# Kernel optimization log

Hardware: AMD Instinct MI355X
Metric: run time of the kernel (lower is better)

## Reference

```python
import jax, jax.numpy as jnp
import numpy as np
from itertools import combinations

NDIM = 256
BATCH = 65536


def setup_inputs() -> dict:
    key = jax.random.key(0)
    k1, k2 = jax.random.split(key)
    pairs = np.array(list(combinations(range(NDIM), 2)), dtype=np.int32)  # [comb(ndim,2), 2]
    return {
        "x": jax.random.normal(k1, (BATCH, NDIM), dtype=jnp.float32),
        "rots": jax.random.normal(k2, (pairs.shape[0],), dtype=jnp.float32),
        "idx_i": jnp.asarray(pairs[:, 0]),
        "idx_j": jnp.asarray(pairs[:, 1]),
    }


def _build_mat(rots, idx_i, idx_j, ndim):
    # Equivalent to mat = R_last @ ... @ R_first @ I, then return mat.T.
    # Each Givens rotation R_(i,j,theta) only mixes rows i and j, so we update
    # two rows per step (O(ndim) work) instead of a dense ndim x ndim matmul.
    # Torch uses cfloat, but all imaginary parts are identically zero, so
    # float32 computes the same math.
    def step(mat, t):
        i, j, theta = t
        c = jnp.cos(theta)
        s = jnp.sin(theta)
        ri = mat[i]
        rj = mat[j]
        mat = mat.at[i].set(c * ri - s * rj)
        mat = mat.at[j].set(s * ri + c * rj)
        return mat, None

    mat0 = jnp.eye(ndim, dtype=rots.dtype)
    mat, _ = jax.lax.scan(step, mat0, (idx_i, idx_j, rots))
    return mat.T  # forward does x @ mat.T


def reference(x, rots, idx_i, idx_j):
    m = _build_mat(rots, idx_i, idx_j, x.shape[-1])  # [ndim, ndim]
    return x @ m
```

## Files before the change

### kernel.cpp

```cpp
#include <hip/hip_runtime.h>
#include <hip/hip_bf16.h>
#include <math.h>

#define NDIM 256
#define NROT 32640
#define NSEG 64
#define SEGLEN 510
#define MATE (NDIM * NDIM)
#define NODEE (2 * MATE)

typedef __bf16 bf16x4_t __attribute__((ext_vector_type(4)));
typedef __bf16 bf16x8_t __attribute__((ext_vector_type(8)));
typedef float f32x4_t __attribute__((ext_vector_type(4)));


#define ROT1(RJ, CS) { float nri_ = fmaf((CS).x, ri, -((CS).y * (RJ))); \
                       (RJ) = fmaf((CS).y, ri, (CS).x * (RJ)); ri = nri_; }

#define LOAD16(P, JB, KK) \
    P##0 = *(const f32x4_t*)&tile[(JB)][t][0]; \
    P##1 = *(const f32x4_t*)&tile[(JB)][t][4]; \
    P##2 = *(const f32x4_t*)&tile[(JB) + 1][t][0]; \
    P##3 = *(const f32x4_t*)&tile[(JB) + 1][t][4]; \
    _Pragma("unroll") \
    for (int u = 0; u < 16; u++) P##c[u] = csl[(KK) + u];

#define COMP16(P, JB) \
    _Pragma("unroll") \
    for (int u = 0; u < 4; u++) ROT1(P##0[u], P##c[u]) \
    _Pragma("unroll") \
    for (int u = 0; u < 4; u++) ROT1(P##1[u], P##c[4 + u]) \
    _Pragma("unroll") \
    for (int u = 0; u < 4; u++) ROT1(P##2[u], P##c[8 + u]) \
    _Pragma("unroll") \
    for (int u = 0; u < 4; u++) ROT1(P##3[u], P##c[12 + u]) \
    *(f32x4_t*)&tile[(JB)][t][0] = P##0; \
    *(f32x4_t*)&tile[(JB)][t][4] = P##1; \
    *(f32x4_t*)&tile[(JB) + 1][t][0] = P##2; \
    *(f32x4_t*)&tile[(JB) + 1][t][4] = P##3;

__global__ __launch_bounds__(64, 1) void k_build(const float* __restrict__ rots,
                                                 __bf16* __restrict__ leaves) {
    __shared__ float tile[32][64][8];
    __shared__ float2 csl[SEGLEN + 16];
    const int t = threadIdx.x;
    const int seg = blockIdx.x >> 2;
    const int cg = blockIdx.x & 3;
    const int col = cg * 64 + t;
    const int kg0 = seg * SEGLEN;

    for (int u = t; u < SEGLEN; u += 64) {
        float th = rots[kg0 + u];
        float s, c;
        sincosf(th, &s, &c);
        csl[u] = make_float2(c, s);
    }
    for (int u = SEGLEN + t; u < SEGLEN + 16; u += 64) csl[u] = make_float2(1.f, 0.f);

    #pragma unroll
    for (int jb = 0; jb < 32; jb++) {
        f32x4_t z0 = {0.f, 0.f, 0.f, 0.f}, z1 = {0.f, 0.f, 0.f, 0.f};
        if ((col >> 3) == jb) {
            if ((col & 7) < 4) z0[col & 3] = 1.0f;
            else               z1[col & 3] = 1.0f;
        }
        *(f32x4_t*)&tile[jb][t][0] = z0;
        *(f32x4_t*)&tile[jb][t][4] = z1;
    }

    int k = 0;
    int i = 0, cum = 0;
    while (cum + (NDIM - 1 - i) <= kg0) { cum += NDIM - 1 - i; i++; }
    int j = i + 1 + (kg0 - cum);

    float* T = &tile[0][0][0];
    #define TADDR(r) ((((r) >> 3) * 512) + t * 8 + ((r) & 7))

    while (k < SEGLEN) {
        float ri = T[TADDR(i)];
        int rem = min(NDIM - j, SEGLEN - k);

        int npeel = min((8 - (j & 7)) & 7, rem);
        for (int u = 0; u < npeel; u++) {
            float2 cs = csl[k];
            float rj = T[TADDR(j)];
            float nri = fmaf(cs.x, ri, -(cs.y * rj));
            T[TADDR(j)] = fmaf(cs.y, ri, cs.x * rj);
            ri = nri; j++; k++;
        }
        rem -= npeel;

        if (rem >= 16) {
            int jb = j >> 3;
            f32x4_t A0, A1, A2, A3, B0, B1, B2, B3;
            float2 Ac[16], Bc[16];
            LOAD16(A, jb, k)
            while (rem >= 48) {
                LOAD16(B, jb + 2, k + 16)
                COMP16(A, jb)
                jb += 2; j += 16; k += 16; rem -= 16;
                LOAD16(A, jb + 2, k + 16)
                COMP16(B, jb)
                jb += 2; j += 16; k += 16; rem -= 16;
            }
            if (rem >= 32) {
                LOAD16(B, jb + 2, k + 16)
                COMP16(A, jb)
                jb += 2; j += 16; k += 16; rem -= 16;
                COMP16(B, jb)
                jb += 2; j += 16; k += 16; rem -= 16;
            } else {
                COMP16(A, jb)
                jb += 2; j += 16; k += 16; rem -= 16;
            }
        }

        if (rem >= 8) {
            int jb = j >> 3;
            f32x4_t a0 = *(const f32x4_t*)&tile[jb][t][0];
            f32x4_t a1 = *(const f32x4_t*)&tile[jb][t][4];
            float2 cc[8];
            #pragma unroll
            for (int u = 0; u < 8; u++) cc[u] = csl[k + u];
            #pragma unroll
            for (int u = 0; u < 4; u++) ROT1(a0[u], cc[u])
            #pragma unroll
            for (int u = 0; u < 4; u++) ROT1(a1[u], cc[4 + u])
            *(f32x4_t*)&tile[jb][t][0] = a0;
            *(f32x4_t*)&tile[jb][t][4] = a1;
            j += 8; k += 8; rem -= 8;
        }

        while (rem > 0) {
            float2 cs = csl[k];
            float rj = T[TADDR(j)];
            float nri = fmaf(cs.x, ri, -(cs.y * rj));
            T[TADDR(j)] = fmaf(cs.y, ri, cs.x * rj);
            ri = nri; j++; k++; rem--;
        }

        T[TADDR(i)] = ri;
        if (j == NDIM) { i++; j = i + 1; }
    }
    #undef TADDR

    __bf16* hi = leaves + (size_t)seg * NODEE;
    __bf16* lo = hi + MATE;
    if (seg & 1) {
        for (int jb = 0; jb < 32; jb++) {
            f32x4_t v0 = *(const f32x4_t*)&tile[jb][t][0];
            f32x4_t v1 = *(const f32x4_t*)&tile[jb][t][4];
            #pragma unroll
            for (int u = 0; u < 8; u++) {
                float v = (u < 4) ? v0[u & 3] : v1[u & 3];
                __bf16 h = (__bf16)v;
                hi[(size_t)(jb * 8 + u) * NDIM + col] = h;
                lo[(size_t)(jb * 8 + u) * NDIM + col] = (__bf16)(v - (float)h);
            }
        }
    } else {
        for (int jb = 0; jb < 32; jb++) {
            f32x4_t v0 = *(const f32x4_t*)&tile[jb][t][0];
            f32x4_t v1 = *(const f32x4_t*)&tile[jb][t][4];
            bf16x8_t vh, vl;
            #pragma unroll
            for (int u = 0; u < 8; u++) {
                float v = (u < 4) ? v0[u & 3] : v1[u & 3];
                __bf16 h = (__bf16)v;
                vh[u] = h;
                vl[u] = (__bf16)(v - (float)h);
            }
            *(bf16x8_t*)&hi[(size_t)col * NDIM + jb * 8] = vh;
            *(bf16x8_t*)&lo[(size_t)col * NDIM + jb * 8] = vl;
        }
    }
}

#define LDK 264
__global__ __launch_bounds__(256) void k_combine(const __bf16* __restrict__ src,
                                                 __bf16* __restrict__ dst,
                                                 int finalLevel) {
    __shared__ __bf16 planes[4][64 * LDK];

    const int p = blockIdx.x >> 4;
    const int qd = blockIdx.x & 15;
    const int rbq = (qd >> 2) * 64;
    const int cbq = (qd & 3) * 64;
    const __bf16* A = src + (size_t)(2 * p) * NODEE;
    const __bf16* B = src + (size_t)(2 * p + 1) * NODEE;
    __bf16* Chi = dst + (size_t)p * NODEE;
    __bf16* Clo = Chi + MATE;
    const bool storeT = (!finalLevel) && ((p & 1) == 0);

    const int t = threadIdx.x;
    const int wid = t >> 6, lane = t & 63;
    const int wr2 = (wid >> 1) * 32, wc2 = (wid & 1) * 32;
    const int lrow = lane & 15, kg = lane >> 4;

    const __bf16* plane_src[4] = {B, B + MATE, A, A + MATE};
    const int plane_row0[4] = {rbq, rbq, cbq, cbq};
    #pragma unroll
    for (int q = 0; q < 32; q++) {
        int g = q * 256 + t;
        int pl = g >> 11;
        int c = g & 2047;
        int row = c >> 5, sg = c & 31;
        bf16x8_t v = *(const bf16x8_t*)&plane_src[pl][(size_t)(plane_row0[pl] + row) * NDIM + sg * 8];
        *(bf16x8_t*)&planes[pl][row * LDK + sg * 8] = v;
    }
    __syncthreads();

    f32x4_t acc[2][2] = {};
    #pragma unroll
    for (int kc = 0; kc < 8; kc++) {
        bf16x8_t afh[2], afl[2], bfh[2], bfl[2];
        #pragma unroll
        for (int mt = 0; mt < 2; mt++) {
            int r = (wr2 + mt * 16 + lrow) * LDK + kc * 32 + kg * 8;
            afh[mt] = *(const bf16x8_t*)&planes[0][r];
            afl[mt] = *(const bf16x8_t*)&planes[1][r];
        }
        #pragma unroll
        for (int nt = 0; nt < 2; nt++) {
            int r = (wc2 + nt * 16 + lrow) * LDK + kc * 32 + kg * 8;
            bfh[nt] = *(const bf16x8_t*)&planes[2][r];
            bfl[nt] = *(const bf16x8_t*)&planes[3][r];
        }
        #pragma unroll
        for (int mt = 0; mt < 2; mt++)
            #pragma unroll
            for (int nt = 0; nt < 2; nt++) {
                acc[mt][nt] = __builtin_amdgcn_mfma_f32_16x16x32_bf16(afh[mt], bfh[nt], acc[mt][nt], 0, 0, 0);
                acc[mt][nt] = __builtin_amdgcn_mfma_f32_16x16x32_bf16(afh[mt], bfl[nt], acc[mt][nt], 0, 0, 0);
                acc[mt][nt] = __builtin_amdgcn_mfma_f32_16x16x32_bf16(afl[mt], bfh[nt], acc[mt][nt], 0, 0, 0);
            }
    }

    #pragma unroll
    for (int mt = 0; mt < 2; mt++)
        #pragma unroll
        for (int nt = 0; nt < 2; nt++) {
            int grow = rbq + wr2 + mt * 16 + kg * 4;
            int gcol = cbq + wc2 + nt * 16 + lrow;
            if (storeT) {
                bf16x4_t vh, vl;
                #pragma unroll
                for (int r = 0; r < 4; r++) {
                    float v = acc[mt][nt][r];
                    __bf16 h = (__bf16)v;
                    vh[r] = h;
                    vl[r] = (__bf16)(v - (float)h);
                }
                *(bf16x4_t*)&Chi[(size_t)gcol * NDIM + grow] = vh;
                *(bf16x4_t*)&Clo[(size_t)gcol * NDIM + grow] = vl;
            } else if (finalLevel) {
                #pragma unroll
                for (int r = 0; r < 4; r++)
                    Chi[(size_t)(grow + r) * NDIM + gcol] = (__bf16)acc[mt][nt][r];
            } else {
                #pragma unroll
                for (int r = 0; r < 4; r++) {
                    float v = acc[mt][nt][r];
                    __bf16 h = (__bf16)v;
                    Chi[(size_t)(grow + r) * NDIM + gcol] = h;
                    Clo[(size_t)(grow + r) * NDIM + gcol] = (__bf16)(v - (float)h);
                }
            }
        }
}

#define LDA 72
__global__ __launch_bounds__(256, 2) void k_gemm(const float* __restrict__ X,
                                                 const __bf16* __restrict__ Mhi,
                                                 float* __restrict__ Y) {
    __shared__ __bf16 As[128 * LDA];
    __shared__ __bf16 Bs[128 * LDA];
    const int bx = blockIdx.x;
    const int xcd = bx & 7;
    const int q = bx >> 3;
    const int bn = (q & 1) * 128;
    const int bm = (xcd + (q >> 1) * 8) * 128;
    const int t = threadIdx.x;
    const int wid = t >> 6;
    const int lane = t & 63;
    const int wr = (wid >> 1) * 64;
    const int wc = (wid & 1) * 64;
    const int lrow = lane & 15;
    const int kg = lane >> 4;

    f32x4_t acc[4][4] = {};

    f32x4_t ra[8];
    bf16x8_t rb[4];

    #pragma unroll
    for (int qq = 0; qq < 8; qq++) {
        int g = qq * 256 + t;
        ra[qq] = *(const f32x4_t*)&X[(size_t)(bm + (g >> 4)) * 256 + (g & 15) * 4];
    }
    #pragma unroll
    for (int qq = 0; qq < 4; qq++) {
        int g = qq * 256 + t;
        rb[qq] = *(const bf16x8_t*)&Mhi[(size_t)(bn + (g >> 3)) * 256 + (g & 7) * 8];
    }

    #pragma unroll
    for (int it = 0; it < 4; it++) {
        #pragma unroll
        for (int qq = 0; qq < 8; qq++) {
            int g = qq * 256 + t;
            f32x4_t v = ra[qq];
            bf16x4_t h = {(__bf16)v.x, (__bf16)v.y, (__bf16)v.z, (__bf16)v.w};
            *(bf16x4_t*)&As[(g >> 4) * LDA + (g & 15) * 4] = h;
        }
        #pragma unroll
        for (int qq = 0; qq < 4; qq++) {
            int g = qq * 256 + t;
            *(bf16x8_t*)&Bs[(g >> 3) * LDA + (g & 7) * 8] = rb[qq];
        }
        __syncthreads();

        if (it < 3) {
            int kc = (it + 1) * 64;
            #pragma unroll
            for (int qq = 0; qq < 8; qq++) {
                int g = qq * 256 + t;
                ra[qq] = *(const f32x4_t*)&X[(size_t)(bm + (g >> 4)) * 256 + kc + (g & 15) * 4];
            }
            #pragma unroll
            for (int qq = 0; qq < 4; qq++) {
                int g = qq * 256 + t;
                rb[qq] = *(const bf16x8_t*)&Mhi[(size_t)(bn + (g >> 3)) * 256 + kc + (g & 7) * 8];
            }
        }

        #pragma unroll
        for (int k2 = 0; k2 < 2; k2++) {
            bf16x8_t af[4], bfr[4];
            #pragma unroll
            for (int mt = 0; mt < 4; mt++)
                af[mt] = *(const bf16x8_t*)&As[(wr + mt * 16 + lrow) * LDA + k2 * 32 + kg * 8];
            #pragma unroll
            for (int nt = 0; nt < 4; nt++)
                bfr[nt] = *(const bf16x8_t*)&Bs[(wc + nt * 16 + lrow) * LDA + k2 * 32 + kg * 8];
            #pragma unroll
            for (int mt = 0; mt < 4; mt++)
                #pragma unroll
                for (int nt = 0; nt < 4; nt++)
                    acc[mt][nt] = __builtin_amdgcn_mfma_f32_16x16x32_bf16(af[mt], bfr[nt], acc[mt][nt], 0, 0, 0);
        }
        __syncthreads();
    }

    const int ocol = bn + wc + lrow;
    const int orow = bm + wr + kg * 4;
    #pragma unroll
    for (int mt = 0; mt < 4; mt++)
        #pragma unroll
        for (int nt = 0; nt < 4; nt++)
            #pragma unroll
            for (int r = 0; r < 4; r++)
                Y[(size_t)(orow + mt * 16 + r) * 256 + ocol + nt * 16] = acc[mt][nt][r];
}

extern "C" void kernel_launch(void* const* d_in, const int* in_sizes, int n_in,
                              void* d_out, int out_size, void* d_ws, size_t ws_size,
                              hipStream_t stream) {
    const float* x = (const float*)d_in[0];
    const float* rots = (const float*)d_in[1];
    float* out = (float*)d_out;

    __bf16* B0 = (__bf16*)d_ws;
    __bf16* B1 = B0 + (size_t)NSEG * NODEE;

    k_build<<<NSEG * 4, 64, 0, stream>>>(rots, B0);
    k_combine<<<32 * 16, 256, 0, stream>>>(B0, B1, 0);
    k_combine<<<16 * 16, 256, 0, stream>>>(B1, B0, 0);
    k_combine<<<8 * 16, 256, 0, stream>>>(B0, B1, 0);
    k_combine<<<4 * 16, 256, 0, stream>>>(B1, B0, 0);
    k_combine<<<2 * 16, 256, 0, stream>>>(B0, B1, 0);
    k_combine<<<1 * 16, 256, 0, stream>>>(B1, B0, 1);
    k_gemm<<<1024, 256, 0, stream>>>(x, B0, out);
}
```

Before: 222.5 us.

## Merge tree combine levels into one cooperative kernel with grid sync

Replaces six separate k_combine launches with a single cooperative kernel of 256 blocks that loops over the tree levels and separates them with grid.sync. The aim is to remove the per-launch overhead and the gaps between small, serial launches in the later levels. In exchange, the first level now runs 512 tiles on 256 blocks, so each block does two tiles in turn. The grid-wide barrier also adds its own cost.

After: 572.5 us. +157.3%, slower.

```diff
diff --git a/kernel.cpp b/kernel.cpp
--- a/kernel.cpp
+++ b/kernel.cpp
@@ -1,6 +1,9 @@
 #include <hip/hip_runtime.h>
 #include <hip/hip_bf16.h>
+#include <hip/hip_cooperative_groups.h>
 #include <math.h>
+
+namespace cg = cooperative_groups;
 
 #define NDIM 256
 #define NROT 32640
@@ -45,8 +48,8 @@
     __shared__ float2 csl[SEGLEN + 16];
     const int t = threadIdx.x;
     const int seg = blockIdx.x >> 2;
-    const int cg = blockIdx.x & 3;
-    const int col = cg * 64 + t;
+    const int cg_ = blockIdx.x & 3;
+    const int col = cg_ * 64 + t;
     const int kg0 = seg * SEGLEN;
 
     for (int u = t; u < SEGLEN; u += 64) {
@@ -177,13 +180,12 @@
 }
 
 #define LDK 264
-__global__ __launch_bounds__(256) void k_combine(const __bf16* __restrict__ src,
-                                                 __bf16* __restrict__ dst,
-                                                 int finalLevel) {
-    __shared__ __bf16 planes[4][64 * LDK];
-
-    const int p = blockIdx.x >> 4;
-    const int qd = blockIdx.x & 15;
+
+__device__ __forceinline__ void combine_tile(int p, int qd,
+                                             const __bf16* __restrict__ src,
+                                             __bf16* __restrict__ dst,
+                                             int finalLevel,
+                                             __bf16 (&planes)[4][64 * LDK]) {
     const int rbq = (qd >> 2) * 64;
     const int cbq = (qd & 3) * 64;
     const __bf16* A = src + (size_t)(2 * p) * NODEE;
@@ -269,6 +271,25 @@
         }
 }
 
+__global__ __launch_bounds__(256, 1) void k_tree(__bf16* B0, __bf16* B1) {
+    __shared__ __bf16 planes[4][64 * LDK];
+    cg::grid_group grid = cg::this_grid();
+
+    #pragma unroll 1
+    for (int lv = 0; lv < 6; lv++) {
+        const __bf16* src = (lv & 1) ? (const __bf16*)B1 : (const __bf16*)B0;
+        __bf16* dst = (lv & 1) ? B0 : B1;
+        const int np = NSEG >> (lv + 1);
+        const int njobs = np * 16;
+        for (int job = blockIdx.x; job < njobs; job += gridDim.x) {
+            combine_tile(job >> 4, job & 15, src, dst, lv == 5, planes);
+            __syncthreads();
+        }
+        __threadfence();
+        grid.sync();
+    }
+}
+
 #define LDA 72
 __global__ __launch_bounds__(256, 2) void k_gemm(const float* __restrict__ X,
                                                  const __bf16* __restrict__ Mhi,
@@ -374,11 +395,9 @@
     __bf16* B1 = B0 + (size_t)NSEG * NODEE;
 
     k_build<<<NSEG * 4, 64, 0, stream>>>(rots, B0);
-    k_combine<<<32 * 16, 256, 0, stream>>>(B0, B1, 0);
-    k_combine<<<16 * 16, 256, 0, stream>>>(B1, B0, 0);
-    k_combine<<<8 * 16, 256, 0, stream>>>(B0, B1, 0);
-    k_combine<<<4 * 16, 256, 0, stream>>>(B1, B0, 0);
-    k_combine<<<2 * 16, 256, 0, stream>>>(B0, B1, 0);
-    k_combine<<<1 * 16, 256, 0, stream>>>(B1, B0, 1);
+
+    void* args[] = {(void*)&B0, (void*)&B1};
+    hipLaunchCooperativeKernel((void*)k_tree, dim3(256), dim3(256), args, 0, stream);
+
     k_gemm<<<1024, 256, 0, stream>>>(x, B0, out);
 }
```

## Restructure final GEMM to keep M half resident in LDS and stream X from global

Applied to the files above, without the earlier changes.

The final x @ M GEMM is rewritten so each 512-thread block loads a 128-column half of the bf16 matrix (all 256 K) into LDS once. Each wave then streams its 32 rows of X straight from global memory into MFMA A-fragments, converting fp32 to bf16 in registers. This drops the per-K-chunk LDS staging of X and the double syncthreads loop. In exchange, X reads are strided 32-byte pieces per lane with no software prefetch, and X is read twice in total because each column half is a separate block. A variable rename in k_build is cosmetic.

Result: no change. 223.5 us (+0.5%).

```diff
diff --git a/kernel.cpp b/kernel.cpp
--- a/kernel.cpp
+++ b/kernel.cpp
@@ -45,8 +45,8 @@
     __shared__ float2 csl[SEGLEN + 16];
     const int t = threadIdx.x;
     const int seg = blockIdx.x >> 2;
-    const int cg = blockIdx.x & 3;
-    const int col = cg * 64 + t;
+    const int cg_ = blockIdx.x & 3;
+    const int col = cg_ * 64 + t;
     const int kg0 = seg * SEGLEN;
 
     for (int u = t; u < SEGLEN; u += 64) {
@@ -269,98 +269,54 @@
         }
 }
 
-#define LDA 72
-__global__ __launch_bounds__(256, 2) void k_gemm(const float* __restrict__ X,
+#define LDM 264
+__global__ __launch_bounds__(512, 1) void k_gemm(const float* __restrict__ X,
                                                  const __bf16* __restrict__ Mhi,
                                                  float* __restrict__ Y) {
-    __shared__ __bf16 As[128 * LDA];
-    __shared__ __bf16 Bs[128 * LDA];
+    __shared__ __bf16 Ms[128 * LDM];
     const int bx = blockIdx.x;
-    const int xcd = bx & 7;
-    const int q = bx >> 3;
-    const int bn = (q & 1) * 128;
-    const int bm = (xcd + (q >> 1) * 8) * 128;
+    const int rg = bx & 255;
+    const int ch = bx >> 8;
     const int t = threadIdx.x;
-    const int wid = t >> 6;
-    const int lane = t & 63;
-    const int wr = (wid >> 1) * 64;
-    const int wc = (wid & 1) * 64;
-    const int lrow = lane & 15;
-    const int kg = lane >> 4;
-
-    f32x4_t acc[4][4] = {};
-
-    f32x4_t ra[8];
-    bf16x8_t rb[4];
-
-    #pragma unroll
-    for (int qq = 0; qq < 8; qq++) {
-        int g = qq * 256 + t;
-        ra[qq] = *(const f32x4_t*)&X[(size_t)(bm + (g >> 4)) * 256 + (g & 15) * 4];
-    }
-    #pragma unroll
-    for (int qq = 0; qq < 4; qq++) {
-        int g = qq * 256 + t;
-        rb[qq] = *(const bf16x8_t*)&Mhi[(size_t)(bn + (g >> 3)) * 256 + (g & 7) * 8];
-    }
-
-    #pragma unroll
-    for (int it = 0; it < 4; it++) {
-        #pragma unroll
-        for (int qq = 0; qq < 8; qq++) {
-            int g = qq * 256 + t;
-            f32x4_t v = ra[qq];
-            bf16x4_t h = {(__bf16)v.x, (__bf16)v.y, (__bf16)v.z, (__bf16)v.w};
-            *(bf16x4_t*)&As[(g >> 4) * LDA + (g & 15) * 4] = h;
-        }
-        #pragma unroll
-        for (int qq = 0; qq < 4; qq++) {
-            int g = qq * 256 + t;
-            *(bf16x8_t*)&Bs[(g >> 3) * LDA + (g & 7) * 8] = rb[qq];
-        }
-        __syncthreads();
-
-        if (it < 3) {
-            int kc = (it + 1) * 64;
-            #pragma unroll
-            for (int qq = 0; qq < 8; qq++) {
-                int g = qq * 256 + t;
-                ra[qq] = *(const f32x4_t*)&X[(size_t)(bm + (g >> 4)) * 256 + kc + (g & 15) * 4];
-            }
-            #pragma unroll
-            for (int qq = 0; qq < 4; qq++) {
-                int g = qq * 256 + t;
-                rb[qq] = *(const bf16x8_t*)&Mhi[(size_t)(bn + (g >> 3)) * 256 + kc + (g & 7) * 8];
-            }
-        }
-
-        #pragma unroll
-        for (int k2 = 0; k2 < 2; k2++) {
-            bf16x8_t af[4], bfr[4];
-            #pragma unroll
-            for (int mt = 0; mt < 4; mt++)
-                af[mt] = *(const bf16x8_t*)&As[(wr + mt * 16 + lrow) * LDA + k2 * 32 + kg * 8];
-            #pragma unroll
-            for (int nt = 0; nt < 4; nt++)
-                bfr[nt] = *(const bf16x8_t*)&Bs[(wc + nt * 16 + lrow) * LDA + k2 * 32 + kg * 8];
-            #pragma unroll
-            for (int mt = 0; mt < 4; mt++)
-                #pragma unroll
-                for (int nt = 0; nt < 4; nt++)
-                    acc[mt][nt] = __builtin_amdgcn_mfma_f32_16x16x32_bf16(af[mt], bfr[nt], acc[mt][nt], 0, 0, 0);
-        }
-        __syncthreads();
-    }
-
-    const int ocol = bn + wc + lrow;
-    const int orow = bm + wr + kg * 4;
-    #pragma unroll
-    for (int mt = 0; mt < 4; mt++)
-        #pragma unroll
-        for (int nt = 0; nt < 4; nt++)
+    const int wid = t >> 6, lane = t & 63;
+    const int lrow = lane & 15, kg = lane >> 4;
+
+    #pragma unroll
+    for (int q = 0; q < 8; q++) {
+        int g = q * 512 + t;
+        int row = g >> 5, sg = g & 31;
+        bf16x8_t v = *(const bf16x8_t*)&Mhi[(size_t)(ch * 128 + row) * 256 + sg * 8];
+        *(bf16x8_t*)&Ms[row * LDM + sg * 8] = v;
+    }
+    __syncthreads();
+
+    const int row0 = rg * 256 + wid * 32;
+    #pragma unroll
+    for (int sl = 0; sl < 2; sl++) {
+        const int rb = row0 + sl * 16;
+        f32x4_t acc[8] = {};
+        #pragma unroll
+        for (int kc = 0; kc < 8; kc++) {
+            const float* xp = &X[(size_t)(rb + lrow) * 256 + kc * 32 + kg * 8];
+            f32x4_t x0 = *(const f32x4_t*)xp;
+            f32x4_t x1 = *(const f32x4_t*)(xp + 4);
+            bf16x8_t af;
+            af[0] = (__bf16)x0.x; af[1] = (__bf16)x0.y;
+            af[2] = (__bf16)x0.z; af[3] = (__bf16)x0.w;
+            af[4] = (__bf16)x1.x; af[5] = (__bf16)x1.y;
+            af[6] = (__bf16)x1.z; af[7] = (__bf16)x1.w;
+            #pragma unroll
+            for (int nt = 0; nt < 8; nt++) {
+                bf16x8_t bf = *(const bf16x8_t*)&Ms[(nt * 16 + lrow) * LDM + kc * 32 + kg * 8];
+                acc[nt] = __builtin_amdgcn_mfma_f32_16x16x32_bf16(af, bf, acc[nt], 0, 0, 0);
+            }
+        }
+        #pragma unroll
+        for (int nt = 0; nt < 8; nt++)
             #pragma unroll
             for (int r = 0; r < 4; r++)
-                Y[(size_t)(orow + mt * 16 + r) * 256 + ocol + nt * 16] = acc[mt][nt][r];
+                Y[(size_t)(rb + kg * 4 + r) * 256 + ch * 128 + nt * 16 + lrow] = acc[nt][r];
+    }
 }
 
 extern "C" void kernel_launch(void* const* d_in, const int* in_sizes, int n_in,
@@ -380,5 +336,5 @@
     k_combine<<<4 * 16, 256, 0, stream>>>(B1, B0, 0);
     k_combine<<<2 * 16, 256, 0, stream>>>(B0, B1, 0);
     k_combine<<<1 * 16, 256, 0, stream>>>(B1, B0, 1);
-    k_gemm<<<1024, 256, 0, stream>>>(x, B0, out);
+    k_gemm<<<512, 512, 0, stream>>>(x, B0, out);
 }
```

## Balance build segments by row cost and split combine K-loop into halves

Applied to the files above, without the earlier changes.

The build kernel now splits rotations into segments on whole-row boundaries, chosen by a cost model (fixed cost per row plus cost per rotation). This removes mid-row segment starts and is meant to even out per-block work. The combine kernel stages K in two halves of 128 with smaller shared memory, prefetching the second half into registers while the first is computed, and allows two blocks per CU. The final GEMM is split into two launches of 512 blocks with a row offset, which adds one launch.

Measured after the change: 217.9 us. -2.1%, faster.

```diff
diff --git a/kernel.cpp b/kernel.cpp
--- a/kernel.cpp
+++ b/kernel.cpp
@@ -5,9 +5,12 @@
 #define NDIM 256
 #define NROT 32640
 #define NSEG 64
-#define SEGLEN 510
 #define MATE (NDIM * NDIM)
 #define NODEE (2 * MATE)
+
+#define BF 1280
+#define BC 16
+#define CSLMAX 1104
 
 typedef __bf16 bf16x4_t __attribute__((ext_vector_type(4)));
 typedef __bf16 bf16x8_t __attribute__((ext_vector_type(8)));
@@ -39,23 +42,45 @@
     *(f32x4_t*)&tile[(JB) + 1][t][0] = P##2; \
     *(f32x4_t*)&tile[(JB) + 1][t][4] = P##3;
 
+__device__ __forceinline__ int run_off(int r) {
+    return 255 * r - (r * (r - 1)) / 2;
+}
+__device__ __forceinline__ int cum_cost(int r) {
+    return BF * r + BC * run_off(r);
+}
+__device__ __forceinline__ int seg_boundary(int s) {
+    if (s <= 0) return 0;
+    if (s >= NSEG) return 255;
+    const long target = ((long)cum_cost(255) * s) / NSEG;
+    int lo = 0, hi = 255;
+    while (lo < hi) {
+        int mid = (lo + hi) >> 1;
+        if ((long)cum_cost(mid) >= target) hi = mid; else lo = mid + 1;
+    }
+    return lo;
+}
+
 __global__ __launch_bounds__(64, 1) void k_build(const float* __restrict__ rots,
                                                  __bf16* __restrict__ leaves) {
     __shared__ float tile[32][64][8];
-    __shared__ float2 csl[SEGLEN + 16];
+    __shared__ float2 csl[CSLMAX];
     const int t = threadIdx.x;
     const int seg = blockIdx.x >> 2;
-    const int cg = blockIdx.x & 3;
-    const int col = cg * 64 + t;
-    const int kg0 = seg * SEGLEN;
-
-    for (int u = t; u < SEGLEN; u += 64) {
+    const int cg_ = blockIdx.x & 3;
+    const int col = cg_ * 64 + t;
+
+    const int r0 = seg_boundary(seg);
+    const int r1 = seg_boundary(seg + 1);
+    const int kg0 = run_off(r0);
+    const int nrot = run_off(r1) - kg0;
+
+    for (int u = t; u < nrot; u += 64) {
         float th = rots[kg0 + u];
         float s, c;
         sincosf(th, &s, &c);
         csl[u] = make_float2(c, s);
     }
-    for (int u = SEGLEN + t; u < SEGLEN + 16; u += 64) csl[u] = make_float2(1.f, 0.f);
+    for (int u = nrot + t; u < nrot + 16 && u < CSLMAX; u += 64) csl[u] = make_float2(1.f, 0.f);
 
     #pragma unroll
     for (int jb = 0; jb < 32; jb++) {
@@ -68,17 +93,14 @@
         *(f32x4_t*)&tile[jb][t][4] = z1;
     }
 
-    int k = 0;
-    int i = 0, cum = 0;
-    while (cum + (NDIM - 1 - i) <= kg0) { cum += NDIM - 1 - i; i++; }
-    int j = i + 1 + (kg0 - cum);
-
     float* T = &tile[0][0][0];
     #define TADDR(r) ((((r) >> 3) * 512) + t * 8 + ((r) & 7))
 
-    while (k < SEGLEN) {
+    int k = 0;
+    for (int i = r0; i < r1; ++i) {
         float ri = T[TADDR(i)];
-        int rem = min(NDIM - j, SEGLEN - k);
+        int j = i + 1;
+        int rem = NDIM - j;
 
         int npeel = min((8 - (j & 7)) & 7, rem);
         for (int u = 0; u < npeel; u++) {
@@ -140,7 +162,6 @@
         }
 
         T[TADDR(i)] = ri;
-        if (j == NDIM) { i++; j = i + 1; }
     }
     #undef TADDR
 
@@ -176,11 +197,11 @@
     }
 }
 
-#define LDK 264
-__global__ __launch_bounds__(256) void k_combine(const __bf16* __restrict__ src,
-                                                 __bf16* __restrict__ dst,
-                                                 int finalLevel) {
-    __shared__ __bf16 planes[4][64 * LDK];
+#define LDK2 136
+__global__ __launch_bounds__(256, 2) void k_combine(const __bf16* __restrict__ src,
+                                                    __bf16* __restrict__ dst,
+                                                    int finalLevel) {
+    __shared__ __bf16 planes[4][64 * LDK2];
 
     const int p = blockIdx.x >> 4;
     const int qd = blockIdx.x & 15;
@@ -199,30 +220,77 @@
 
     const __bf16* plane_src[4] = {B, B + MATE, A, A + MATE};
     const int plane_row0[4] = {rbq, rbq, cbq, cbq};
-    #pragma unroll
-    for (int q = 0; q < 32; q++) {
+
+    #pragma unroll
+    for (int q = 0; q < 16; q++) {
         int g = q * 256 + t;
-        int pl = g >> 11;
-        int c = g & 2047;
-        int row = c >> 5, sg = c & 31;
+        int pl = g >> 10;
+        int c = g & 1023;
+        int row = c >> 4, sg = c & 15;
         bf16x8_t v = *(const bf16x8_t*)&plane_src[pl][(size_t)(plane_row0[pl] + row) * NDIM + sg * 8];
-        *(bf16x8_t*)&planes[pl][row * LDK + sg * 8] = v;
+        *(bf16x8_t*)&planes[pl][row * LDK2 + sg * 8] = v;
     }
     __syncthreads();
 
+    bf16x8_t pre[16];
+    #pragma unroll
+    for (int q = 0; q < 16; q++) {
+        int g = q * 256 + t;
+        int pl = g >> 10;
+        int c = g & 1023;
+        int row = c >> 4, sg = c & 15;
+        pre[q] = *(const bf16x8_t*)&plane_src[pl][(size_t)(plane_row0[pl] + row) * NDIM + 128 + sg * 8];
+    }
+
     f32x4_t acc[2][2] = {};
     #pragma unroll
-    for (int kc = 0; kc < 8; kc++) {
+    for (int kc = 0; kc < 4; kc++) {
         bf16x8_t afh[2], afl[2], bfh[2], bfl[2];
         #pragma unroll
         for (int mt = 0; mt < 2; mt++) {
-            int r = (wr2 + mt * 16 + lrow) * LDK + kc * 32 + kg * 8;
+            int r = (wr2 + mt * 16 + lrow) * LDK2 + kc * 32 + kg * 8;
             afh[mt] = *(const bf16x8_t*)&planes[0][r];
             afl[mt] = *(const bf16x8_t*)&planes[1][r];
         }
         #pragma unroll
         for (int nt = 0; nt < 2; nt++) {
-            int r = (wc2 + nt * 16 + lrow) * LDK + kc * 32 + kg * 8;
+            int r = (wc2 + nt * 16 + lrow) * LDK2 + kc * 32 + kg * 8;
+            bfh[nt] = *(const bf16x8_t*)&planes[2][r];
+            bfl[nt] = *(const bf16x8_t*)&planes[3][r];
+        }
+        #pragma unroll
+        for (int mt = 0; mt < 2; mt++)
+            #pragma unroll
+            for (int nt = 0; nt < 2; nt++) {
+                acc[mt][nt] = __builtin_amdgcn_mfma_f32_16x16x32_bf16(afh[mt], bfh[nt], acc[mt][nt], 0, 0, 0);
+                acc[mt][nt] = __builtin_amdgcn_mfma_f32_16x16x32_bf16(afh[mt], bfl[nt], acc[mt][nt], 0, 0, 0);
+                acc[mt][nt] = __builtin_amdgcn_mfma_f32_16x16x32_bf16(afl[mt], bfh[nt], acc[mt][nt], 0, 0, 0);
+            }
+    }
+    __syncthreads();
+
+    #pragma unroll
+    for (int q = 0; q < 16; q++) {
+        int g = q * 256 + t;
+        int pl = g >> 10;
+        int c = g & 1023;
+        int row = c >> 4, sg = c & 15;
+        *(bf16x8_t*)&planes[pl][row * LDK2 + sg * 8] = pre[q];
+    }
+    __syncthreads();
+
+    #pragma unroll
+    for (int kc = 0; kc < 4; kc++) {
+        bf16x8_t afh[2], afl[2], bfh[2], bfl[2];
+        #pragma unroll
+        for (int mt = 0; mt < 2; mt++) {
+            int r = (wr2 + mt * 16 + lrow) * LDK2 + kc * 32 + kg * 8;
+            afh[mt] = *(const bf16x8_t*)&planes[0][r];
+            afl[mt] = *(const bf16x8_t*)&planes[1][r];
+        }
+        #pragma unroll
+        for (int nt = 0; nt < 2; nt++) {
+            int r = (wc2 + nt * 16 + lrow) * LDK2 + kc * 32 + kg * 8;
             bfh[nt] = *(const bf16x8_t*)&planes[2][r];
             bfl[nt] = *(const bf16x8_t*)&planes[3][r];
         }
@@ -272,14 +340,15 @@
 #define LDA 72
 __global__ __launch_bounds__(256, 2) void k_gemm(const float* __restrict__ X,
                                                  const __bf16* __restrict__ Mhi,
-                                                 float* __restrict__ Y) {
+                                                 float* __restrict__ Y,
+                                                 int rowOff) {
     __shared__ __bf16 As[128 * LDA];
     __shared__ __bf16 Bs[128 * LDA];
     const int bx = blockIdx.x;
     const int xcd = bx & 7;
     const int q = bx >> 3;
     const int bn = (q & 1) * 128;
-    const int bm = (xcd + (q >> 1) * 8) * 128;
+    const int bm = (xcd + (q >> 1) * 8) * 128 + rowOff;
     const int t = threadIdx.x;
     const int wid = t >> 6;
     const int lane = t & 63;
@@ -380,5 +449,6 @@
     k_combine<<<4 * 16, 256, 0, stream>>>(B1, B0, 0);
     k_combine<<<2 * 16, 256, 0, stream>>>(B0, B1, 0);
     k_combine<<<1 * 16, 256, 0, stream>>>(B1, B0, 1);
-    k_gemm<<<1024, 256, 0, stream>>>(x, B0, out);
-}
+    k_gemm<<<512, 256, 0, stream>>>(x, B0, out, 0);
+    k_gemm<<<512, 256, 0, stream>>>(x, B0, out, 32768);
+}
```
